# Kernel tuning notes

Hardware: AMD Instinct MI355X
Metric: run time of the kernel (lower is better)

Reference implementation:

```python
import jax, jax.numpy as jnp
import numpy as np

NUM_NODES = 100000
NUM_EDGES = 1600000
D = 128

def sage_conv(x, src, dst, Wl, bl, Wr):
    # PyG SAGEConv (mean aggr): out = lin_l(mean_{j->i} x_j) + lin_r(x_i)
    msgs = x[src]                                            # [E, D] gather
    agg = jax.ops.segment_sum(msgs, dst, num_segments=x.shape[0])  # [N, D]
    deg = jax.ops.segment_sum(jnp.ones((src.shape[0],), x.dtype), dst,
                              num_segments=x.shape[0])       # [N]
    mean = agg / jnp.maximum(deg, 1.0)[:, None]
    return mean @ Wl.T + bl + x @ Wr.T

def setup_inputs() -> dict:
    key = jax.random.key(0)
    ks = jax.random.split(key, 16)
    s = 1.0 / np.sqrt(D)
    inp = {
        'x': jax.random.randint(ks[0], (NUM_NODES, 1), 0, NUM_NODES),
        'edge_index': jax.random.randint(ks[1], (2, NUM_EDGES), 0, NUM_NODES),
        'batch': jnp.zeros((NUM_NODES,), dtype=jnp.int64),
        'item_emb': jax.random.normal(ks[2], (NUM_NODES, D), jnp.float32),
        'edge_emb': jax.random.normal(ks[3], (NUM_EDGES, D), jnp.float32),
        'Wl1': jax.random.uniform(ks[4], (D, D), jnp.float32, -s, s),
        'bl1': jnp.zeros((D,), jnp.float32),
        'Wr1': jax.random.uniform(ks[5], (D, D), jnp.float32, -s, s),
        'Wl2': jax.random.uniform(ks[6], (D, D), jnp.float32, -s, s),
        'bl2': jnp.zeros((D,), jnp.float32),
        'Wr2': jax.random.uniform(ks[7], (D, D), jnp.float32, -s, s),
        'Wl3': jax.random.uniform(ks[8], (D, D), jnp.float32, -s, s),
        'bl3': jnp.zeros((D,), jnp.float32),
        'Wr3': jax.random.uniform(ks[9], (D, D), jnp.float32, -s, s),
        'W_lin1': jax.random.uniform(ks[10], (D, D), jnp.float32, -s, s),
        'b_lin1': jnp.zeros((D,), jnp.float32),
        'W_lin2': jax.random.uniform(ks[11], (D, D), jnp.float32, -s, s),
        'b_lin2': jnp.zeros((D,), jnp.float32),
    }
    return inp

def reference(x, edge_index, batch, item_emb, edge_emb,
              Wl1, bl1, Wr1, Wl2, bl2, Wr2, Wl3, bl3, Wr3,
              W_lin1, b_lin1, W_lin2, b_lin2):
    src, dst = edge_index[0], edge_index[1]
    h = item_emb[x[:, 0]]                      # embedding lookup + squeeze(1) -> [N, D]
    e = edge_emb                               # edge_embedding(arange(E)) == full table
    h = jax.nn.relu(sage_conv(h, src, dst, Wl1, bl1, Wr1))
    h = jax.nn.relu(sage_conv(h, src, dst, Wl2, bl2, Wr2))
    h = jax.nn.relu(sage_conv(h, src, dst, Wl3, bl3, Wr3))
    h = jax.nn.relu(h @ W_lin1.T + b_lin1)     # dropout is identity in eval mode
    e_out = jax.nn.relu(e @ W_lin2.T + b_lin2)
    return h, e_out
```

## Files before the change

kernel.cpp:

```cpp
#include <hip/hip_runtime.h>

#define NN  100000
#define NNP 100096
#define NE  1600000
#define DD  128

typedef __attribute__((ext_vector_type(8))) short bf16x8;
typedef __attribute__((ext_vector_type(4))) float f32x4;

__device__ __forceinline__ float bf2f(unsigned short u){
  union { unsigned int i; float f; } v; v.i = ((unsigned int)u) << 16; return v.f;
}
__device__ __forceinline__ unsigned short f2bf(float f){
  union { float f; unsigned int i; } v; v.f = f;
  unsigned int u = v.i;
  return (unsigned short)((u + 0x7fffu + ((u >> 16) & 1u)) >> 16);
}
__device__ __forceinline__ unsigned int cvt_pk_bf16(float lo, float hi){
  unsigned int r;
  asm("v_cvt_pk_bf16_f32 %0, %1, %2" : "=v"(r) : "v"(lo), "v"(hi));
  return r;
}

struct WPtrs { const float* w[8]; };
__global__ __launch_bounds__(256) void cvt_w_all(WPtrs wp, unsigned short* __restrict__ o){
  int t = blockIdx.x * 256 + threadIdx.x;
  int m = t >> 13, i = t & 8191;
  float2 v = ((const float2*)wp.w[m])[i];
  ((unsigned int*)o)[t] = cvt_pk_bf16(v.x, v.y);
}

__global__ __launch_bounds__(256) void count_deg(const int* __restrict__ dst,
                                                 int* __restrict__ deg, int n){
  int t = blockIdx.x * 256 + threadIdx.x;
  if (t < n) atomicAdd(&deg[dst[t]], 1);
}

#define SCAN_CHUNK 1024
__global__ __launch_bounds__(256) void partial_sums(const int* __restrict__ deg,
                                                    int* __restrict__ partials, int n){
  __shared__ int lds[256];
  int t = threadIdx.x;
  int base = blockIdx.x * SCAN_CHUNK + t * 4;
  int s = 0;
  #pragma unroll
  for (int i = 0; i < 4; ++i){ int idx = base + i; s += (idx < n) ? deg[idx] : 0; }
  lds[t] = s; __syncthreads();
  for (int off = 128; off > 0; off >>= 1){
    if (t < off) lds[t] += lds[t + off];
    __syncthreads();
  }
  if (t == 0) partials[blockIdx.x] = lds[0];
}

__global__ void scan_partials(int* partials, int nb){
  if (threadIdx.x == 0 && blockIdx.x == 0){
    int acc = 0;
    for (int i = 0; i < nb; ++i){ int v = partials[i]; partials[i] = acc; acc += v; }
  }
}

__global__ __launch_bounds__(256) void scan_block(const int* __restrict__ deg,
                                                  const int* __restrict__ partials,
                                                  int* __restrict__ row_start, int n){
  __shared__ int lds[256];
  int t = threadIdx.x;
  int base = blockIdx.x * SCAN_CHUNK + t * 4;
  int v[4]; int s = 0;
  #pragma unroll
  for (int i = 0; i < 4; ++i){ int idx = base + i; v[i] = (idx < n) ? deg[idx] : 0; s += v[i]; }
  lds[t] = s; __syncthreads();
  for (int off = 1; off < 256; off <<= 1){
    int x = (t >= off) ? lds[t - off] : 0;
    __syncthreads();
    lds[t] += x;
    __syncthreads();
  }
  int excl = ((t == 0) ? 0 : lds[t - 1]) + partials[blockIdx.x];
  #pragma unroll
  for (int i = 0; i < 4; ++i){ int idx = base + i; if (idx < n) row_start[idx] = excl; excl += v[i]; }
}

__global__ __launch_bounds__(256) void fill_csr(const int* __restrict__ src,
                                                const int* __restrict__ dst,
                                                const int* __restrict__ row_start,
                                                int* __restrict__ cursor,
                                                int* __restrict__ csr, int n){
  int t = blockIdx.x * 256 + threadIdx.x;
  if (t < n){
    int d = dst[t];
    int pos = atomicAdd(&cursor[d], 1);
    csr[row_start[d] + pos] = src[t];
  }
}

__global__ __launch_bounds__(256) void gather_h0(const int* __restrict__ x,
                                                 const float* __restrict__ emb,
                                                 unsigned short* __restrict__ h, int n){
  int t = blockIdx.x * 256 + threadIdx.x;
  if (t >= n * 64) return;
  int node = t >> 6, p = t & 63;
  int s = x[node];
  float2 v = *(const float2*)(emb + (size_t)s * DD + p * 2);
  ((unsigned int*)h)[t] = cvt_pk_bf16(v.x, v.y);
}

__global__ __launch_bounds__(256) void aggregate2(const unsigned short* __restrict__ h,
                                                  const int* __restrict__ csr,
                                                  const int* __restrict__ row_start,
                                                  const int* __restrict__ deg,
                                                  unsigned short* __restrict__ mean, int n){
  int node = blockIdx.x * 4 + (threadIdx.x >> 6);
  if (node >= n) return;
  int lane = threadIdx.x & 63;
  int st = row_start[node];
  int d = deg[node];
  const unsigned int* hp = (const unsigned int*)h;
  float s0 = 0.f, s1 = 0.f, t0 = 0.f, t1 = 0.f;
  float u0 = 0.f, u1 = 0.f, w0 = 0.f, w1 = 0.f;
  int i = 0;
  for (; i + 4 <= d; i += 4){
    int n0 = csr[st + i], n1 = csr[st + i + 1], n2 = csr[st + i + 2], n3 = csr[st + i + 3];
    unsigned int v0 = hp[(size_t)n0 * 64 + lane];
    unsigned int v1 = hp[(size_t)n1 * 64 + lane];
    unsigned int v2 = hp[(size_t)n2 * 64 + lane];
    unsigned int v3 = hp[(size_t)n3 * 64 + lane];
    s0 += bf2f((unsigned short)(v0 & 0xffffu)); s1 += bf2f((unsigned short)(v0 >> 16));
    t0 += bf2f((unsigned short)(v1 & 0xffffu)); t1 += bf2f((unsigned short)(v1 >> 16));
    u0 += bf2f((unsigned short)(v2 & 0xffffu)); u1 += bf2f((unsigned short)(v2 >> 16));
    w0 += bf2f((unsigned short)(v3 & 0xffffu)); w1 += bf2f((unsigned short)(v3 >> 16));
  }
  for (; i < d; ++i){
    int s = csr[st + i];
    unsigned int v = hp[(size_t)s * 64 + lane];
    s0 += bf2f((unsigned short)(v & 0xffffu)); s1 += bf2f((unsigned short)(v >> 16));
  }
  s0 += t0 + u0 + w0;
  s1 += t1 + u1 + w1;
  float inv = 1.0f / fmaxf((float)d, 1.0f);
  ((unsigned int*)mean)[(size_t)node * 64 + lane] = cvt_pk_bf16(s0 * inv, s1 * inv);
}

__device__ __forceinline__ void stage_mat(const unsigned short* __restrict__ Bg,
                                          unsigned short* sB){
  int t = threadIdx.x;
  #pragma unroll
  for (int it = 0; it < 8; ++it){
    int idx = it * 256 + t;
    int kc = idx >> 7, col = idx & 127;
    uint4 v = *(const uint4*)(Bg + (size_t)col * DD + kc * 8);
    *(uint4*)(sB + (size_t)idx * 8) = v;
  }
}

__global__ __launch_bounds__(256) void gemm_edge2(
    const float* __restrict__ A, const unsigned short* __restrict__ Bg,
    const float* __restrict__ bias, float* __restrict__ out, int ntiles)
{
  __shared__ unsigned short sB[16384];
  stage_mat(Bg, sB);
  __syncthreads();
  int wave = threadIdx.x >> 6, lane = threadIdx.x & 63;
  int lr = lane & 15, lk = lane >> 4;
  float bv[8];
  #pragma unroll
  for (int j = 0; j < 8; ++j) bv[j] = bias[j * 16 + lr];

  for (int tile = blockIdx.x; tile < ntiles; tile += gridDim.x){
    size_t r0 = (size_t)tile * 128 + wave * 32;
    const float* Ap = A + (r0 + lr) * DD + lk * 8;
    bf16x8 a[2][4];
    #pragma unroll
    for (int g = 0; g < 2; ++g){
      #pragma unroll
      for (int ks = 0; ks < 4; ++ks){
        f32x4 a0 = *(const f32x4*)(Ap + (size_t)g * 16 * DD + ks * 32);
        f32x4 a1 = *(const f32x4*)(Ap + (size_t)g * 16 * DD + ks * 32 + 4);
        union { bf16x8 v; unsigned int u[4]; } au;
        au.u[0] = cvt_pk_bf16(a0[0], a0[1]);
        au.u[1] = cvt_pk_bf16(a0[2], a0[3]);
        au.u[2] = cvt_pk_bf16(a1[0], a1[1]);
        au.u[3] = cvt_pk_bf16(a1[2], a1[3]);
        a[g][ks] = au.v;
      }
    }
    f32x4 acc[2][8];
    #pragma unroll
    for (int g = 0; g < 2; ++g)
      #pragma unroll
      for (int j = 0; j < 8; ++j) acc[g][j] = (f32x4){0.f, 0.f, 0.f, 0.f};
    #pragma unroll
    for (int ks = 0; ks < 4; ++ks){
      #pragma unroll
      for (int j = 0; j < 8; ++j){
        bf16x8 b = *(const bf16x8*)(sB + ((ks * 4 + lk) * 128 + j * 16 + lr) * 8);
        acc[0][j] = __builtin_amdgcn_mfma_f32_16x16x32_bf16(a[0][ks], b, acc[0][j], 0, 0, 0);
        acc[1][j] = __builtin_amdgcn_mfma_f32_16x16x32_bf16(a[1][ks], b, acc[1][j], 0, 0, 0);
      }
    }
    #pragma unroll
    for (int g = 0; g < 2; ++g)
      #pragma unroll
      for (int j = 0; j < 8; ++j)
        #pragma unroll
        for (int r = 0; r < 4; ++r){
          size_t row = r0 + g * 16 + lk * 4 + r;
          out[row * DD + j * 16 + lr] = fmaxf(acc[g][j][r] + bv[j], 0.f);
        }
  }
}

template<int DUAL, int OUTF32>
__global__ __launch_bounds__(256) void gemm_node2(
    const unsigned short* __restrict__ A1, const unsigned short* __restrict__ B1g,
    const unsigned short* __restrict__ A2, const unsigned short* __restrict__ B2g,
    const float* __restrict__ bias, void* __restrict__ outp, int M, int ntiles)
{
  __shared__ unsigned short sB[DUAL ? 32768 : 16384];
  stage_mat(B1g, sB);
  if (DUAL) stage_mat(B2g, sB + 16384);
  __syncthreads();
  int wave = threadIdx.x >> 6, lane = threadIdx.x & 63;
  int lr = lane & 15, lk = lane >> 4;
  float bv[8];
  #pragma unroll
  for (int j = 0; j < 8; ++j) bv[j] = bias[j * 16 + lr];

  for (int tile = blockIdx.x; tile < ntiles; tile += gridDim.x){
    size_t r0 = (size_t)tile * 128 + wave * 32;
    f32x4 acc[2][8];
    #pragma unroll
    for (int g = 0; g < 2; ++g)
      #pragma unroll
      for (int j = 0; j < 8; ++j) acc[g][j] = (f32x4){0.f, 0.f, 0.f, 0.f};

    {
      const unsigned short* Ap = A1 + (r0 + lr) * DD + lk * 8;
      bf16x8 a[2][4];
      #pragma unroll
      for (int g = 0; g < 2; ++g)
        #pragma unroll
        for (int ks = 0; ks < 4; ++ks)
          a[g][ks] = *(const bf16x8*)(Ap + (size_t)g * 16 * DD + ks * 32);
      #pragma unroll
      for (int ks = 0; ks < 4; ++ks){
        #pragma unroll
        for (int j = 0; j < 8; ++j){
          bf16x8 b = *(const bf16x8*)(sB + ((ks * 4 + lk) * 128 + j * 16 + lr) * 8);
          acc[0][j] = __builtin_amdgcn_mfma_f32_16x16x32_bf16(a[0][ks], b, acc[0][j], 0, 0, 0);
          acc[1][j] = __builtin_amdgcn_mfma_f32_16x16x32_bf16(a[1][ks], b, acc[1][j], 0, 0, 0);
        }
      }
    }
    if (DUAL){
      const unsigned short* Ap = A2 + (r0 + lr) * DD + lk * 8;
      bf16x8 a[2][4];
      #pragma unroll
      for (int g = 0; g < 2; ++g)
        #pragma unroll
        for (int ks = 0; ks < 4; ++ks)
          a[g][ks] = *(const bf16x8*)(Ap + (size_t)g * 16 * DD + ks * 32);
      #pragma unroll
      for (int ks = 0; ks < 4; ++ks){
        #pragma unroll
        for (int j = 0; j < 8; ++j){
          bf16x8 b = *(const bf16x8*)(sB + 16384 + ((ks * 4 + lk) * 128 + j * 16 + lr) * 8);
          acc[0][j] = __builtin_amdgcn_mfma_f32_16x16x32_bf16(a[0][ks], b, acc[0][j], 0, 0, 0);
          acc[1][j] = __builtin_amdgcn_mfma_f32_16x16x32_bf16(a[1][ks], b, acc[1][j], 0, 0, 0);
        }
      }
    }
    #pragma unroll
    for (int g = 0; g < 2; ++g)
      #pragma unroll
      for (int j = 0; j < 8; ++j)
        #pragma unroll
        for (int r = 0; r < 4; ++r){
          size_t row = r0 + g * 16 + lk * 4 + r;
          float v = fmaxf(acc[g][j][r] + bv[j], 0.f);
          if (OUTF32){
            if (row < (size_t)M) ((float*)outp)[row * DD + j * 16 + lr] = v;
          } else {
            ((unsigned short*)outp)[row * DD + j * 16 + lr] = f2bf(v);
          }
        }
  }
}

extern "C" void kernel_launch(void* const* d_in, const int* in_sizes, int n_in,
                              void* d_out, int out_size, void* d_ws, size_t ws_size,
                              hipStream_t stream)
{
  const int*   x    = (const int*)d_in[0];
  const int*   ei   = (const int*)d_in[1];
  const int*   srcp = ei;
  const int*   dstp = ei + NE;
  const float* item = (const float*)d_in[3];
  const float* eemb = (const float*)d_in[4];
  WPtrs wp;
  wp.w[0] = (const float*)d_in[5];
  wp.w[1] = (const float*)d_in[7];
  wp.w[2] = (const float*)d_in[8];
  wp.w[3] = (const float*)d_in[10];
  wp.w[4] = (const float*)d_in[11];
  wp.w[5] = (const float*)d_in[13];
  wp.w[6] = (const float*)d_in[14];
  wp.w[7] = (const float*)d_in[16];
  const float* bl1 = (const float*)d_in[6];
  const float* bl2 = (const float*)d_in[9];
  const float* bl3 = (const float*)d_in[12];
  const float* bq1 = (const float*)d_in[15];
  const float* bq2 = (const float*)d_in[17];

  char* ws = (char*)d_ws;
  size_t o = 0;
  auto alloc = [&](size_t bytes) -> void* {
    void* p = ws + o;
    o += (bytes + 255) & ~(size_t)255;
    return p;
  };
  unsigned short* wbf      = (unsigned short*)alloc(8 * 16384 * 2);
  int*            deg      = (int*)alloc((size_t)NN * 4);
  int*            cursor   = (int*)alloc((size_t)NN * 4);
  int*            row_st   = (int*)alloc((size_t)NN * 4);
  int*            partials = (int*)alloc(4096);
  int*            csr      = (int*)alloc((size_t)NE * 4);
  unsigned short* mean     = (unsigned short*)alloc((size_t)NNP * DD * 2);
  unsigned short* h_a      = (unsigned short*)alloc((size_t)NNP * DD * 2);
  unsigned short* h_b      = (unsigned short*)alloc((size_t)NNP * DD * 2);

  float* out_h = (float*)d_out;
  float* out_e = out_h + (size_t)NN * DD;

  hipMemsetAsync(deg, 0, (((size_t)NN * 4 + 255) & ~(size_t)255) * 2, stream);

  cvt_w_all<<<256, 256, 0, stream>>>(wp, wbf);

  const int nb = (NN + SCAN_CHUNK - 1) / SCAN_CHUNK;
  count_deg<<<(NE + 255) / 256, 256, 0, stream>>>(dstp, deg, NE);
  partial_sums<<<nb, 256, 0, stream>>>(deg, partials, NN);
  scan_partials<<<1, 64, 0, stream>>>(partials, nb);
  scan_block<<<nb, 256, 0, stream>>>(deg, partials, row_st, NN);
  fill_csr<<<(NE + 255) / 256, 256, 0, stream>>>(srcp, dstp, row_st, cursor, csr, NE);

  gather_h0<<<(NN * 64 + 255) / 256, 256, 0, stream>>>(x, item, h_a, NN);

  const int agg_grid   = (NN + 3) / 4;
  const int node_tiles = NNP / 128;
  const int edge_tiles = NE / 128;

  aggregate2<<<agg_grid, 256, 0, stream>>>(h_a, csr, row_st, deg, mean, NN);
  gemm_node2<1,0><<<node_tiles, 256, 0, stream>>>(mean, wbf + 0*16384, h_a, wbf + 1*16384, bl1, h_b, NN, node_tiles);
  aggregate2<<<agg_grid, 256, 0, stream>>>(h_b, csr, row_st, deg, mean, NN);
  gemm_node2<1,0><<<node_tiles, 256, 0, stream>>>(mean, wbf + 2*16384, h_b, wbf + 3*16384, bl2, h_a, NN, node_tiles);
  aggregate2<<<agg_grid, 256, 0, stream>>>(h_a, csr, row_st, deg, mean, NN);
  gemm_node2<1,0><<<node_tiles, 256, 0, stream>>>(mean, wbf + 4*16384, h_a, wbf + 5*16384, bl3, h_b, NN, node_tiles);

  gemm_node2<0,1><<<node_tiles, 256, 0, stream>>>(h_b, wbf + 6*16384, h_b, wbf + 6*16384, bq1, out_h, NN, node_tiles);

  gemm_edge2<<<2500, 256, 0, stream>>>(eemb, wbf + 7*16384, bq2, out_e, edge_tiles);
}
```

Measured before the change: 864.6 us.

## Split edge GEMM into chunks and co-schedule with CSR and node GEMM kernels

The standalone edge-embedding GEMM is removed. Its 12500 tiles are split into chunks of five tiles, and extra blocks run those chunks inside the count_deg, fill_csr and four node GEMM launches. The aim is to overlap the bandwidth-heavy edge GEMM with the atomic-bound CSR build and the small node GEMMs, which leave the GPU underused, and to save one launch. In exchange, the CSR kernels now reserve 32KB of LDS, which may lower their occupancy, and the atomic kernels must compete with the streaming GEMM for memory bandwidth.

Measured after the change: 836.1 us. 1.03x faster.

```diff
diff --git a/kernel.cpp b/kernel.cpp
--- a/kernel.cpp
+++ b/kernel.cpp
@@ -30,10 +30,106 @@
   ((unsigned int*)o)[t] = cvt_pk_bf16(v.x, v.y);
 }
 
-__global__ __launch_bounds__(256) void count_deg(const int* __restrict__ dst,
-                                                 int* __restrict__ deg, int n){
-  int t = blockIdx.x * 256 + threadIdx.x;
+__device__ __forceinline__ void stage_mat(const unsigned short* __restrict__ Bg,
+                                          unsigned short* sB){
+  int t = threadIdx.x;
+  #pragma unroll
+  for (int it = 0; it < 8; ++it){
+    int idx = it * 256 + t;
+    int kc = idx >> 7, col = idx & 127;
+    uint4 v = *(const uint4*)(Bg + (size_t)col * DD + kc * 8);
+    *(uint4*)(sB + (size_t)idx * 8) = v;
+  }
+}
+
+__device__ __forceinline__ void edge_run(const float* __restrict__ A,
+    const unsigned short* __restrict__ Wg, const float* __restrict__ bias,
+    float* __restrict__ out, unsigned short* sB, int tile0, int cnt)
+{
+  stage_mat(Wg, sB);
+  __syncthreads();
+  int wave = threadIdx.x >> 6, lane = threadIdx.x & 63;
+  int lr = lane & 15, lk = lane >> 4;
+  float bv[8];
+  #pragma unroll
+  for (int j = 0; j < 8; ++j) bv[j] = bias[j * 16 + lr];
+
+  for (int t = 0; t < cnt; ++t){
+    size_t r0 = (size_t)(tile0 + t) * 128 + (size_t)wave * 32;
+    const float* Ap = A + (r0 + lr) * DD + lk * 8;
+    bf16x8 a[2][4];
+    #pragma unroll
+    for (int g = 0; g < 2; ++g){
+      #pragma unroll
+      for (int ks = 0; ks < 4; ++ks){
+        f32x4 a0 = *(const f32x4*)(Ap + (size_t)g * 16 * DD + ks * 32);
+        f32x4 a1 = *(const f32x4*)(Ap + (size_t)g * 16 * DD + ks * 32 + 4);
+        union { bf16x8 v; unsigned int u[4]; } au;
+        au.u[0] = cvt_pk_bf16(a0[0], a0[1]);
+        au.u[1] = cvt_pk_bf16(a0[2], a0[3]);
+        au.u[2] = cvt_pk_bf16(a1[0], a1[1]);
+        au.u[3] = cvt_pk_bf16(a1[2], a1[3]);
+        a[g][ks] = au.v;
+      }
+    }
+    f32x4 acc[2][8];
+    #pragma unroll
+    for (int g = 0; g < 2; ++g)
+      #pragma unroll
+      for (int j = 0; j < 8; ++j) acc[g][j] = (f32x4){0.f, 0.f, 0.f, 0.f};
+    #pragma unroll
+    for (int ks = 0; ks < 4; ++ks){
+      #pragma unroll
+      for (int j = 0; j < 8; ++j){
+        bf16x8 b = *(const bf16x8*)(sB + ((ks * 4 + lk) * 128 + j * 16 + lr) * 8);
+        acc[0][j] = __builtin_amdgcn_mfma_f32_16x16x32_bf16(a[0][ks], b, acc[0][j], 0, 0, 0);
+        acc[1][j] = __builtin_amdgcn_mfma_f32_16x16x32_bf16(a[1][ks], b, acc[1][j], 0, 0, 0);
+      }
+    }
+    #pragma unroll
+    for (int g = 0; g < 2; ++g)
+      #pragma unroll
+      for (int j = 0; j < 8; ++j)
+        #pragma unroll
+        for (int r = 0; r < 4; ++r){
+          size_t row = r0 + g * 16 + lk * 4 + r;
+          out[row * DD + j * 16 + lr] = fmaxf(acc[g][j][r] + bv[j], 0.f);
+        }
+  }
+}
+
+#define EDGE_ARGS const float* __restrict__ eA, const unsigned short* __restrict__ eW, \
+                  const float* __restrict__ eBias, float* __restrict__ eOut, \
+                  int eTileBase, int eBlocks
+#define EDGE_PASS eA, eW, eBias, eOut
+#define EDGE_CHUNK 5
+
+__global__ __launch_bounds__(256) void countdeg_edge(
+    const int* __restrict__ dst, int* __restrict__ deg, int n, EDGE_ARGS){
+  __shared__ unsigned short sB[16384];
+  if ((int)blockIdx.x < eBlocks){
+    edge_run(EDGE_PASS, sB, eTileBase + blockIdx.x * EDGE_CHUNK, EDGE_CHUNK);
+    return;
+  }
+  int t = (blockIdx.x - eBlocks) * 256 + threadIdx.x;
   if (t < n) atomicAdd(&deg[dst[t]], 1);
+}
+
+__global__ __launch_bounds__(256) void fillcsr_edge(
+    const int* __restrict__ src, const int* __restrict__ dst,
+    const int* __restrict__ row_start, int* __restrict__ cursor,
+    int* __restrict__ csr, int n, EDGE_ARGS){
+  __shared__ unsigned short sB[16384];
+  if ((int)blockIdx.x < eBlocks){
+    edge_run(EDGE_PASS, sB, eTileBase + blockIdx.x * EDGE_CHUNK, EDGE_CHUNK);
+    return;
+  }
+  int t = (blockIdx.x - eBlocks) * 256 + threadIdx.x;
+  if (t < n){
+    int d = dst[t];
+    int pos = atomicAdd(&cursor[d], 1);
+    csr[row_start[d] + pos] = src[t];
+  }
 }
 
 #define SCAN_CHUNK 1024
@@ -79,19 +175,6 @@
   int excl = ((t == 0) ? 0 : lds[t - 1]) + partials[blockIdx.x];
   #pragma unroll
   for (int i = 0; i < 4; ++i){ int idx = base + i; if (idx < n) row_start[idx] = excl; excl += v[i]; }
-}
-
-__global__ __launch_bounds__(256) void fill_csr(const int* __restrict__ src,
-                                                const int* __restrict__ dst,
-                                                const int* __restrict__ row_start,
-                                                int* __restrict__ cursor,
-                                                int* __restrict__ csr, int n){
-  int t = blockIdx.x * 256 + threadIdx.x;
-  if (t < n){
-    int d = dst[t];
-    int pos = atomicAdd(&cursor[d], 1);
-    csr[row_start[d] + pos] = src[t];
-  }
 }
 
 __global__ __launch_bounds__(256) void gather_h0(const int* __restrict__ x,
@@ -141,82 +224,18 @@
   ((unsigned int*)mean)[(size_t)node * 64 + lane] = cvt_pk_bf16(s0 * inv, s1 * inv);
 }
 
-__device__ __forceinline__ void stage_mat(const unsigned short* __restrict__ Bg,
-                                          unsigned short* sB){
-  int t = threadIdx.x;
-  #pragma unroll
-  for (int it = 0; it < 8; ++it){
-    int idx = it * 256 + t;
-    int kc = idx >> 7, col = idx & 127;
-    uint4 v = *(const uint4*)(Bg + (size_t)col * DD + kc * 8);
-    *(uint4*)(sB + (size_t)idx * 8) = v;
-  }
-}
-
-__global__ __launch_bounds__(256) void gemm_edge2(
-    const float* __restrict__ A, const unsigned short* __restrict__ Bg,
-    const float* __restrict__ bias, float* __restrict__ out, int ntiles)
-{
-  __shared__ unsigned short sB[16384];
-  stage_mat(Bg, sB);
-  __syncthreads();
-  int wave = threadIdx.x >> 6, lane = threadIdx.x & 63;
-  int lr = lane & 15, lk = lane >> 4;
-  float bv[8];
-  #pragma unroll
-  for (int j = 0; j < 8; ++j) bv[j] = bias[j * 16 + lr];
-
-  for (int tile = blockIdx.x; tile < ntiles; tile += gridDim.x){
-    size_t r0 = (size_t)tile * 128 + wave * 32;
-    const float* Ap = A + (r0 + lr) * DD + lk * 8;
-    bf16x8 a[2][4];
-    #pragma unroll
-    for (int g = 0; g < 2; ++g){
-      #pragma unroll
-      for (int ks = 0; ks < 4; ++ks){
-        f32x4 a0 = *(const f32x4*)(Ap + (size_t)g * 16 * DD + ks * 32);
-        f32x4 a1 = *(const f32x4*)(Ap + (size_t)g * 16 * DD + ks * 32 + 4);
-        union { bf16x8 v; unsigned int u[4]; } au;
-        au.u[0] = cvt_pk_bf16(a0[0], a0[1]);
-        au.u[1] = cvt_pk_bf16(a0[2], a0[3]);
-        au.u[2] = cvt_pk_bf16(a1[0], a1[1]);
-        au.u[3] = cvt_pk_bf16(a1[2], a1[3]);
-        a[g][ks] = au.v;
-      }
-    }
-    f32x4 acc[2][8];
-    #pragma unroll
-    for (int g = 0; g < 2; ++g)
-      #pragma unroll
-      for (int j = 0; j < 8; ++j) acc[g][j] = (f32x4){0.f, 0.f, 0.f, 0.f};
-    #pragma unroll
-    for (int ks = 0; ks < 4; ++ks){
-      #pragma unroll
-      for (int j = 0; j < 8; ++j){
-        bf16x8 b = *(const bf16x8*)(sB + ((ks * 4 + lk) * 128 + j * 16 + lr) * 8);
-        acc[0][j] = __builtin_amdgcn_mfma_f32_16x16x32_bf16(a[0][ks], b, acc[0][j], 0, 0, 0);
-        acc[1][j] = __builtin_amdgcn_mfma_f32_16x16x32_bf16(a[1][ks], b, acc[1][j], 0, 0, 0);
-      }
-    }
-    #pragma unroll
-    for (int g = 0; g < 2; ++g)
-      #pragma unroll
-      for (int j = 0; j < 8; ++j)
-        #pragma unroll
-        for (int r = 0; r < 4; ++r){
-          size_t row = r0 + g * 16 + lk * 4 + r;
-          out[row * DD + j * 16 + lr] = fmaxf(acc[g][j][r] + bv[j], 0.f);
-        }
-  }
-}
-
 template<int DUAL, int OUTF32>
-__global__ __launch_bounds__(256) void gemm_node2(
+__global__ __launch_bounds__(256) void node_edge(
     const unsigned short* __restrict__ A1, const unsigned short* __restrict__ B1g,
     const unsigned short* __restrict__ A2, const unsigned short* __restrict__ B2g,
-    const float* __restrict__ bias, void* __restrict__ outp, int M, int ntiles)
+    const float* __restrict__ bias, void* __restrict__ outp, int M,
+    EDGE_ARGS)
 {
   __shared__ unsigned short sB[DUAL ? 32768 : 16384];
+  if ((int)blockIdx.x < eBlocks){
+    edge_run(EDGE_PASS, sB, eTileBase + blockIdx.x * EDGE_CHUNK, EDGE_CHUNK);
+    return;
+  }
   stage_mat(B1g, sB);
   if (DUAL) stage_mat(B2g, sB + 16384);
   __syncthreads();
@@ -226,65 +245,64 @@
   #pragma unroll
   for (int j = 0; j < 8; ++j) bv[j] = bias[j * 16 + lr];
 
-  for (int tile = blockIdx.x; tile < ntiles; tile += gridDim.x){
-    size_t r0 = (size_t)tile * 128 + wave * 32;
-    f32x4 acc[2][8];
+  int tile = blockIdx.x - eBlocks;
+  size_t r0 = (size_t)tile * 128 + wave * 32;
+  f32x4 acc[2][8];
+  #pragma unroll
+  for (int g = 0; g < 2; ++g)
+    #pragma unroll
+    for (int j = 0; j < 8; ++j) acc[g][j] = (f32x4){0.f, 0.f, 0.f, 0.f};
+
+  {
+    const unsigned short* Ap = A1 + (r0 + lr) * DD + lk * 8;
+    bf16x8 a[2][4];
     #pragma unroll
     for (int g = 0; g < 2; ++g)
       #pragma unroll
-      for (int j = 0; j < 8; ++j) acc[g][j] = (f32x4){0.f, 0.f, 0.f, 0.f};
-
-    {
-      const unsigned short* Ap = A1 + (r0 + lr) * DD + lk * 8;
-      bf16x8 a[2][4];
-      #pragma unroll
-      for (int g = 0; g < 2; ++g)
-        #pragma unroll
-        for (int ks = 0; ks < 4; ++ks)
-          a[g][ks] = *(const bf16x8*)(Ap + (size_t)g * 16 * DD + ks * 32);
-      #pragma unroll
-      for (int ks = 0; ks < 4; ++ks){
-        #pragma unroll
-        for (int j = 0; j < 8; ++j){
-          bf16x8 b = *(const bf16x8*)(sB + ((ks * 4 + lk) * 128 + j * 16 + lr) * 8);
-          acc[0][j] = __builtin_amdgcn_mfma_f32_16x16x32_bf16(a[0][ks], b, acc[0][j], 0, 0, 0);
-          acc[1][j] = __builtin_amdgcn_mfma_f32_16x16x32_bf16(a[1][ks], b, acc[1][j], 0, 0, 0);
+      for (int ks = 0; ks < 4; ++ks)
+        a[g][ks] = *(const bf16x8*)(Ap + (size_t)g * 16 * DD + ks * 32);
+    #pragma unroll
+    for (int ks = 0; ks < 4; ++ks){
+      #pragma unroll
+      for (int j = 0; j < 8; ++j){
+        bf16x8 b = *(const bf16x8*)(sB + ((ks * 4 + lk) * 128 + j * 16 + lr) * 8);
+        acc[0][j] = __builtin_amdgcn_mfma_f32_16x16x32_bf16(a[0][ks], b, acc[0][j], 0, 0, 0);
+        acc[1][j] = __builtin_amdgcn_mfma_f32_16x16x32_bf16(a[1][ks], b, acc[1][j], 0, 0, 0);
+      }
+    }
+  }
+  if (DUAL){
+    const unsigned short* Ap = A2 + (r0 + lr) * DD + lk * 8;
+    bf16x8 a[2][4];
+    #pragma unroll
+    for (int g = 0; g < 2; ++g)
+      #pragma unroll
+      for (int ks = 0; ks < 4; ++ks)
+        a[g][ks] = *(const bf16x8*)(Ap + (size_t)g * 16 * DD + ks * 32);
+    #pragma unroll
+    for (int ks = 0; ks < 4; ++ks){
+      #pragma unroll
+      for (int j = 0; j < 8; ++j){
+        bf16x8 b = *(const bf16x8*)(sB + 16384 + ((ks * 4 + lk) * 128 + j * 16 + lr) * 8);
+        acc[0][j] = __builtin_amdgcn_mfma_f32_16x16x32_bf16(a[0][ks], b, acc[0][j], 0, 0, 0);
+        acc[1][j] = __builtin_amdgcn_mfma_f32_16x16x32_bf16(a[1][ks], b, acc[1][j], 0, 0, 0);
+      }
+    }
+  }
+  #pragma unroll
+  for (int g = 0; g < 2; ++g)
+    #pragma unroll
+    for (int j = 0; j < 8; ++j)
+      #pragma unroll
+      for (int r = 0; r < 4; ++r){
+        size_t row = r0 + g * 16 + lk * 4 + r;
+        float v = fmaxf(acc[g][j][r] + bv[j], 0.f);
+        if (OUTF32){
+          if (row < (size_t)M) ((float*)outp)[row * DD + j * 16 + lr] = v;
+        } else {
+          ((unsigned short*)outp)[row * DD + j * 16 + lr] = f2bf(v);
         }
       }
-    }
-    if (DUAL){
-      const unsigned short* Ap = A2 + (r0 + lr) * DD + lk * 8;
-      bf16x8 a[2][4];
-      #pragma unroll
-      for (int g = 0; g < 2; ++g)
-        #pragma unroll
-        for (int ks = 0; ks < 4; ++ks)
-          a[g][ks] = *(const bf16x8*)(Ap + (size_t)g * 16 * DD + ks * 32);
-      #pragma unroll
-      for (int ks = 0; ks < 4; ++ks){
-        #pragma unroll
-        for (int j = 0; j < 8; ++j){
-          bf16x8 b = *(const bf16x8*)(sB + 16384 + ((ks * 4 + lk) * 128 + j * 16 + lr) * 8);
-          acc[0][j] = __builtin_amdgcn_mfma_f32_16x16x32_bf16(a[0][ks], b, acc[0][j], 0, 0, 0);
-          acc[1][j] = __builtin_amdgcn_mfma_f32_16x16x32_bf16(a[1][ks], b, acc[1][j], 0, 0, 0);
-        }
-      }
-    }
-    #pragma unroll
-    for (int g = 0; g < 2; ++g)
-      #pragma unroll
-      for (int j = 0; j < 8; ++j)
-        #pragma unroll
-        for (int r = 0; r < 4; ++r){
-          size_t row = r0 + g * 16 + lk * 4 + r;
-          float v = fmaxf(acc[g][j][r] + bv[j], 0.f);
-          if (OUTF32){
-            if (row < (size_t)M) ((float*)outp)[row * DD + j * 16 + lr] = v;
-          } else {
-            ((unsigned short*)outp)[row * DD + j * 16 + lr] = f2bf(v);
-          }
-        }
-  }
 }
 
 extern "C" void kernel_launch(void* const* d_in, const int* in_sizes, int n_in,
@@ -320,9 +338,9 @@
     return p;
   };
   unsigned short* wbf      = (unsigned short*)alloc(8 * 16384 * 2);
-  int*            deg      = (int*)alloc((size_t)NN * 4);
-  int*            cursor   = (int*)alloc((size_t)NN * 4);
-  int*            row_st   = (int*)alloc((size_t)NN * 4);
+  int*            deg      = (int*)alloc((size_t)NNP * 4);
+  int*            cursor   = (int*)alloc((size_t)NNP * 4);
+  int*            row_st   = (int*)alloc((size_t)NNP * 4);
   int*            partials = (int*)alloc(4096);
   int*            csr      = (int*)alloc((size_t)NE * 4);
   unsigned short* mean     = (unsigned short*)alloc((size_t)NNP * DD * 2);
@@ -331,32 +349,41 @@
 
   float* out_h = (float*)d_out;
   float* out_e = out_h + (size_t)NN * DD;
-
-  hipMemsetAsync(deg, 0, (((size_t)NN * 4 + 255) & ~(size_t)255) * 2, stream);
+  const unsigned short* eW = wbf + 7 * 16384;
+
+  hipMemsetAsync(deg, 0, (size_t)NNP * 4 * 2, stream);
 
   cvt_w_all<<<256, 256, 0, stream>>>(wp, wbf);
 
+  int eb = 0;
+  const int e_cd = 250, e_fc = 250, e_nd = 500, e_fin = 500;
+
   const int nb = (NN + SCAN_CHUNK - 1) / SCAN_CHUNK;
-  count_deg<<<(NE + 255) / 256, 256, 0, stream>>>(dstp, deg, NE);
+  const int csr_blk = (NE + 255) / 256;
+
+  countdeg_edge<<<e_cd + csr_blk, 256, 0, stream>>>(dstp, deg, NE,
+      eemb, eW, bq2, out_e, eb * EDGE_CHUNK, e_cd); eb += e_cd;
   partial_sums<<<nb, 256, 0, stream>>>(deg, partials, NN);
   scan_partials<<<1, 64, 0, stream>>>(partials, nb);
   scan_block<<<nb, 256, 0, stream>>>(deg, partials, row_st, NN);
-  fill_csr<<<(NE + 255) / 256, 256, 0, stream>>>(srcp, dstp, row_st, cursor, csr, NE);
+  fillcsr_edge<<<e_fc + csr_blk, 256, 0, stream>>>(srcp, dstp, row_st, cursor, csr, NE,
+      eemb, eW, bq2, out_e, eb * EDGE_CHUNK, e_fc); eb += e_fc;
 
   gather_h0<<<(NN * 64 + 255) / 256, 256, 0, stream>>>(x, item, h_a, NN);
 
   const int agg_grid   = (NN + 3) / 4;
   const int node_tiles = NNP / 128;
-  const int edge_tiles = NE / 128;
 
   aggregate2<<<agg_grid, 256, 0, stream>>>(h_a, csr, row_st, deg, mean, NN);
-  gemm_node2<1,0><<<node_tiles, 256, 0, stream>>>(mean, wbf + 0*16384, h_a, wbf + 1*16384, bl1, h_b, NN, node_tiles);
+  node_edge<1,0><<<e_nd + node_tiles, 256, 0, stream>>>(mean, wbf + 0*16384, h_a, wbf + 1*16384,
+      bl1, h_b, NN, eemb, eW, bq2, out_e, eb * EDGE_CHUNK, e_nd); eb += e_nd;
   aggregate2<<<agg_grid, 256, 0, stream>>>(h_b, csr, row_st, deg, mean, NN);
-  gemm_node2<1,0><<<node_tiles, 256, 0, stream>>>(mean, wbf + 2*16384, h_b, wbf + 3*16384, bl2, h_a, NN, node_tiles);
+  node_edge<1,0><<<e_nd + node_tiles, 256, 0, stream>>>(mean, wbf + 2*16384, h_b, wbf + 3*16384,
+      bl2, h_a, NN, eemb, eW, bq2, out_e, eb * EDGE_CHUNK, e_nd); eb += e_nd;
   aggregate2<<<agg_grid, 256, 0, stream>>>(h_a, csr, row_st, deg, mean, NN);
-  gemm_node2<1,0><<<node_tiles, 256, 0, stream>>>(mean, wbf + 4*16384, h_a, wbf + 5*16384, bl3, h_b, NN, node_tiles);
-
-  gemm_node2<0,1><<<node_tiles, 256, 0, stream>>>(h_b, wbf + 6*16384, h_b, wbf + 6*16384, bq1, out_h, NN, node_tiles);
-
-  gemm_edge2<<<2500, 256, 0, stream>>>(eemb, wbf + 7*16384, bq2, out_e, edge_tiles);
-}
+  node_edge<1,0><<<e_nd + node_tiles, 256, 0, stream>>>(mean, wbf + 4*16384, h_a, wbf + 5*16384,
+      bl3, h_b, NN, eemb, eW, bq2, out_e, eb * EDGE_CHUNK, e_nd); eb += e_nd;
+
+  node_edge<0,1><<<e_fin + node_tiles, 256, 0, stream>>>(h_b, wbf + 6*16384, h_b, wbf + 6*16384,
+      bq1, out_h, NN, eemb, eW, bq2, out_e, eb * EDGE_CHUNK, e_fin); eb += e_fin;
+}
```
